# Kernel tuning notes

Hardware: AMD Instinct MI355X
Metric: run time of the kernel (lower is better)

Reference implementation:

```python
import jax, jax.numpy as jnp
import numpy as np

N = 50000      # nodes
E = 800000     # directed edges (avg degree 16)
D_IN = 128
D_HID = 128


def setup_inputs() -> dict:
    key = jax.random.key(0)
    k = jax.random.split(key, 6)
    x = jax.random.normal(k[0], (N, D_IN), dtype=jnp.float32)
    edge_index = jax.random.randint(k[1], (2, E), 0, N, dtype=jnp.int32)
    s = 1.0 / np.sqrt(D_IN)
    W1 = jax.random.normal(k[2], (D_IN, D_HID), dtype=jnp.float32) * s
    b1 = jnp.zeros((D_HID,), dtype=jnp.float32)
    W2 = jax.random.normal(k[3], (D_HID, D_HID), dtype=jnp.float32) * s
    b2 = jnp.zeros((D_HID,), dtype=jnp.float32)
    return {"x": x, "edge_index": edge_index, "W1": W1, "b1": b1, "W2": W2, "b2": b2}


def reference(x, edge_index, W1, b1, W2, b2):
    # PyG GCNConv default: add self-loops, symmetric normalization.
    src, dst = edge_index[0], edge_index[1]
    loop = jnp.arange(N, dtype=edge_index.dtype)
    s = jnp.concatenate([src, loop])   # [E+N] message sources
    d = jnp.concatenate([dst, loop])   # [E+N] message targets
    # degree on target nodes (incl. self-loops), edge weights = 1
    deg = jax.ops.segment_sum(jnp.ones_like(s, dtype=x.dtype), d, num_segments=N)
    dis = jnp.where(deg > 0, jax.lax.rsqrt(deg), 0.0)
    norm = dis[s] * dis[d]             # [E+N]

    def gcn_conv(h, W, b):
        h = h @ W                                           # [N, D]
        msg = h[s] * norm[:, None]                          # gather + per-edge scale
        return jax.ops.segment_sum(msg, d, num_segments=N) + b  # scatter-add + bias

    h = jax.nn.relu(gcn_conv(x, W1, b1))
    return gcn_conv(h, W2, b2)
```

## Files before the change

kernel.cpp:

```cpp
#include <hip/hip_runtime.h>

#define D 128
#define GBM 64
#define GBK 32


__global__ void k_count(const int* __restrict__ dst, int* __restrict__ cnt, int e) {
    int i = blockIdx.x * blockDim.x + threadIdx.x;
    if (i < e) atomicAdd(&cnt[dst[i]], 1);
}

__global__ __launch_bounds__(256) void k_scan1(const int* __restrict__ cnt,
                                               int* __restrict__ row_ptr,
                                               int* __restrict__ bsum,
                                               float* __restrict__ dis, int n) {
    __shared__ int s[256];
    int i = blockIdx.x * 256 + threadIdx.x;
    int v = (i < n) ? cnt[i] : 0;
    if (i < n) dis[i] = rsqrtf(1.0f + (float)v);
    s[threadIdx.x] = v;
    __syncthreads();
    for (int o = 1; o < 256; o <<= 1) {
        int t = (threadIdx.x >= o) ? s[threadIdx.x - o] : 0;
        __syncthreads();
        s[threadIdx.x] += t;
        __syncthreads();
    }
    if (i < n) row_ptr[i] = s[threadIdx.x] - v;
    if (threadIdx.x == 255) bsum[blockIdx.x] = s[255];
}

__global__ __launch_bounds__(256) void k_scan2(int* __restrict__ bsum, int nb) {
    __shared__ int s[256];
    int v = (threadIdx.x < nb) ? bsum[threadIdx.x] : 0;
    s[threadIdx.x] = v;
    __syncthreads();
    for (int o = 1; o < 256; o <<= 1) {
        int t = (threadIdx.x >= o) ? s[threadIdx.x - o] : 0;
        __syncthreads();
        s[threadIdx.x] += t;
        __syncthreads();
    }
    if (threadIdx.x < nb) bsum[threadIdx.x] = s[threadIdx.x] - v;
}

__global__ void k_scan3(int* __restrict__ row_ptr, const int* __restrict__ bsum, int n) {
    int i = blockIdx.x * 256 + threadIdx.x;
    if (i < n) row_ptr[i] += bsum[blockIdx.x];
}

__global__ void k_place(const int* __restrict__ ei, const int* __restrict__ row_ptr,
                        int* __restrict__ fill, int* __restrict__ srcs, int e) {
    int i = blockIdx.x * blockDim.x + threadIdx.x;
    if (i < e) {
        int s_ = ei[i];
        int d_ = ei[e + i];
        int pos = row_ptr[d_] + atomicAdd(&fill[d_], 1);
        srcs[pos] = s_;
    }
}


__global__ __launch_bounds__(256) void k_gemm_scale(
    const float* __restrict__ X, const float* __restrict__ W,
    const float* __restrict__ dis, float* __restrict__ Y, int nrows) {
    __shared__ float sA[GBK][GBM + 4];
    __shared__ float sB[GBK][D];
    int tid = threadIdx.x;
    int tx = tid & 15;
    int ty = tid >> 4;
    int row0 = blockIdx.x * GBM;

    float acc[4][8] = {};

    for (int kc = 0; kc < D; kc += GBK) {
        __syncthreads();
        #pragma unroll
        for (int jj = 0; jj < 2; ++jj) {
            int i = tid + jj * 256;
            int r = i >> 3;
            int kq = i & 7;
            int gr = row0 + r;
            float4 v = make_float4(0.f, 0.f, 0.f, 0.f);
            if (gr < nrows) v = *(const float4*)(X + (size_t)gr * D + kc + kq * 4);
            sA[kq * 4 + 0][r] = v.x;
            sA[kq * 4 + 1][r] = v.y;
            sA[kq * 4 + 2][r] = v.z;
            sA[kq * 4 + 3][r] = v.w;
        }
        #pragma unroll
        for (int jj = 0; jj < 4; ++jj) {
            int i = tid + jj * 256;
            int k = i >> 5;
            int nq = i & 31;
            *(float4*)(&sB[k][nq * 4]) = *(const float4*)(W + (size_t)(kc + k) * D + nq * 4);
        }
        __syncthreads();
        #pragma unroll
        for (int k = 0; k < GBK; ++k) {
            float a[4], b[8];
            *(float4*)&a[0] = *(float4*)&sA[k][ty * 4];
            *(float4*)&b[0] = *(float4*)&sB[k][tx * 4];
            *(float4*)&b[4] = *(float4*)&sB[k][tx * 4 + 64];
            #pragma unroll
            for (int i = 0; i < 4; ++i)
                #pragma unroll
                for (int j2 = 0; j2 < 8; ++j2)
                    acc[i][j2] += a[i] * b[j2];
        }
    }
    #pragma unroll
    for (int i = 0; i < 4; ++i) {
        int gr = row0 + ty * 4 + i;
        if (gr < nrows) {
            float dv = dis[gr];
            float4 o0, o1;
            o0.x = acc[i][0] * dv; o0.y = acc[i][1] * dv;
            o0.z = acc[i][2] * dv; o0.w = acc[i][3] * dv;
            o1.x = acc[i][4] * dv; o1.y = acc[i][5] * dv;
            o1.z = acc[i][6] * dv; o1.w = acc[i][7] * dv;
            *(float4*)(Y + (size_t)gr * D + tx * 4) = o0;
            *(float4*)(Y + (size_t)gr * D + tx * 4 + 64) = o1;
        }
    }
}


template <bool RELU>
__global__ __launch_bounds__(256) void k_aggregate(
    const float* __restrict__ g, const int* __restrict__ row_ptr,
    const int* __restrict__ cnt, const int* __restrict__ srcs,
    const float* __restrict__ dis, const float* __restrict__ b,
    float* __restrict__ out, int n) {
    long tid = (long)blockIdx.x * blockDim.x + threadIdx.x;
    int lane = (int)(tid & 31);
    int v = (int)(tid >> 5);
    if (v >= n) return;
    int beg = row_ptr[v];
    int c = cnt[v];
    const float4* g4 = (const float4*)g;
    float4 s0 = g4[(size_t)v * 32 + lane];
    float4 a0 = make_float4(0.f, 0.f, 0.f, 0.f);
    float4 a1 = a0, a2 = a0, a3 = a0;
    int j = 0;
    for (; j + 4 <= c; j += 4) {
        int u0 = srcs[beg + j + 0];
        int u1 = srcs[beg + j + 1];
        int u2 = srcs[beg + j + 2];
        int u3 = srcs[beg + j + 3];
        float4 t0 = g4[(size_t)u0 * 32 + lane];
        float4 t1 = g4[(size_t)u1 * 32 + lane];
        float4 t2 = g4[(size_t)u2 * 32 + lane];
        float4 t3 = g4[(size_t)u3 * 32 + lane];
        a0.x += t0.x; a0.y += t0.y; a0.z += t0.z; a0.w += t0.w;
        a1.x += t1.x; a1.y += t1.y; a1.z += t1.z; a1.w += t1.w;
        a2.x += t2.x; a2.y += t2.y; a2.z += t2.z; a2.w += t2.w;
        a3.x += t3.x; a3.y += t3.y; a3.z += t3.z; a3.w += t3.w;
    }
    for (; j < c; ++j) {
        int u = srcs[beg + j];
        float4 t = g4[(size_t)u * 32 + lane];
        a0.x += t.x; a0.y += t.y; a0.z += t.z; a0.w += t.w;
    }
    float4 acc;
    acc.x = s0.x + (a0.x + a1.x) + (a2.x + a3.x);
    acc.y = s0.y + (a0.y + a1.y) + (a2.y + a3.y);
    acc.z = s0.z + (a0.z + a1.z) + (a2.z + a3.z);
    acc.w = s0.w + (a0.w + a1.w) + (a2.w + a3.w);
    float dv = dis[v];
    float4 bb = ((const float4*)b)[lane];
    acc.x = acc.x * dv + bb.x;
    acc.y = acc.y * dv + bb.y;
    acc.z = acc.z * dv + bb.z;
    acc.w = acc.w * dv + bb.w;
    if (RELU) {
        acc.x = fmaxf(acc.x, 0.f);
        acc.y = fmaxf(acc.y, 0.f);
        acc.z = fmaxf(acc.z, 0.f);
        acc.w = fmaxf(acc.w, 0.f);
    }
    ((float4*)out)[(size_t)v * 32 + lane] = acc;
}


extern "C" void kernel_launch(void* const* d_in, const int* in_sizes, int n_in,
                              void* d_out, int out_size, void* d_ws, size_t ws_size,
                              hipStream_t stream) {
    const float* x  = (const float*)d_in[0];
    const int*   ei = (const int*)d_in[1];
    const float* W1 = (const float*)d_in[2];
    const float* b1 = (const float*)d_in[3];
    const float* W2 = (const float*)d_in[4];
    const float* b2 = (const float*)d_in[5];
    float* out = (float*)d_out;
    int n = in_sizes[0] / D;
    int e = in_sizes[1] / 2;

    char* p = (char*)d_ws;
    auto alloc = [&](size_t bytes) -> char* {
        char* r = p;
        p += (bytes + 255) & ~(size_t)255;
        return r;
    };
    int* cnt     = (int*)alloc((size_t)n * 4);
    int* fill    = (int*)alloc((size_t)n * 4);
    int* row_ptr = (int*)alloc((size_t)n * 4);
    int* bsum    = (int*)alloc(1024);
    float* dis   = (float*)alloc((size_t)n * 4);
    int* srcs    = (int*)alloc((size_t)e * 4);
    float* bufA  = (float*)alloc((size_t)n * D * 4);
    float* bufB  = (float*)alloc((size_t)n * D * 4);

    hipMemsetAsync(cnt, 0, (size_t)n * 4, stream);
    hipMemsetAsync(fill, 0, (size_t)n * 4, stream);

    int nb = (n + 255) / 256;
    k_count<<<(e + 255) / 256, 256, 0, stream>>>(ei + e, cnt, e);
    k_scan1<<<nb, 256, 0, stream>>>(cnt, row_ptr, bsum, dis, n);
    k_scan2<<<1, 256, 0, stream>>>(bsum, nb);
    k_scan3<<<nb, 256, 0, stream>>>(row_ptr, bsum, n);
    k_place<<<(e + 255) / 256, 256, 0, stream>>>(ei, row_ptr, fill, srcs, e);

    int gemm_blocks = (n + GBM - 1) / GBM;
    int agg_blocks = (int)(((long)n * 32 + 255) / 256);

    k_gemm_scale<<<gemm_blocks, 256, 0, stream>>>(x, W1, dis, bufA, n);
    k_aggregate<true><<<agg_blocks, 256, 0, stream>>>(bufA, row_ptr, cnt, srcs, dis, b1, bufB, n);
    k_gemm_scale<<<gemm_blocks, 256, 0, stream>>>(bufB, W2, dis, bufA, n);
    k_aggregate<false><<<agg_blocks, 256, 0, stream>>>(bufA, row_ptr, cnt, srcs, dis, b2, out, n);
}
```

Baseline: 343.2 us.

## Prefetch GEMM tiles in registers, fold scan fixup, widen aggregate unroll

Several unrelated changes at once. The GEMM now prefetches the next K-chunk of X and W into registers while the current chunk is computed, and gets a launch-bounds occupancy hint. The third scan kernel is dropped, so block offsets are added on the fly in placement and aggregation. The two memsets are merged into one, and the aggregate kernel unrolls by 8 with two accumulators and writes its output with nontemporal stores. Together these aim to hide GEMM load latency, remove two launches, and put more gathers in flight, at the cost of higher register pressure and an extra bsum read per node.

```diff
diff --git a/kernel.cpp b/kernel.cpp
--- a/kernel.cpp
+++ b/kernel.cpp
@@ -3,6 +3,8 @@
 #define D 128
 #define GBM 64
 #define GBK 32
+
+typedef float f32x4 __attribute__((ext_vector_type(4)));
 
 
 __global__ void k_count(const int* __restrict__ dst, int* __restrict__ cnt, int e) {
@@ -44,24 +46,20 @@
     if (threadIdx.x < nb) bsum[threadIdx.x] = s[threadIdx.x] - v;
 }
 
-__global__ void k_scan3(int* __restrict__ row_ptr, const int* __restrict__ bsum, int n) {
-    int i = blockIdx.x * 256 + threadIdx.x;
-    if (i < n) row_ptr[i] += bsum[blockIdx.x];
-}
-
 __global__ void k_place(const int* __restrict__ ei, const int* __restrict__ row_ptr,
+                        const int* __restrict__ bsum,
                         int* __restrict__ fill, int* __restrict__ srcs, int e) {
     int i = blockIdx.x * blockDim.x + threadIdx.x;
     if (i < e) {
         int s_ = ei[i];
         int d_ = ei[e + i];
-        int pos = row_ptr[d_] + atomicAdd(&fill[d_], 1);
+        int pos = row_ptr[d_] + bsum[d_ >> 8] + atomicAdd(&fill[d_], 1);
         srcs[pos] = s_;
     }
 }
 
 
-__global__ __launch_bounds__(256) void k_gemm_scale(
+__global__ __launch_bounds__(256, 4) void k_gemm_scale(
     const float* __restrict__ X, const float* __restrict__ W,
     const float* __restrict__ dis, float* __restrict__ Y, int nrows) {
     __shared__ float sA[GBK][GBM + 4];
@@ -71,31 +69,49 @@
     int ty = tid >> 4;
     int row0 = blockIdx.x * GBM;
 
+    int ar  = tid >> 3;
+    int akq = tid & 7;
+    int bk  = tid >> 5;
+    int bnq = tid & 31;
+
+    float4 ra0, ra1, rb0, rb1, rb2, rb3;
+    int gr0 = row0 + ar, gr1 = row0 + ar + 32;
+
+    ra0 = make_float4(0.f, 0.f, 0.f, 0.f); ra1 = ra0;
+    if (gr0 < nrows) ra0 = *(const float4*)(X + (size_t)gr0 * D + akq * 4);
+    if (gr1 < nrows) ra1 = *(const float4*)(X + (size_t)gr1 * D + akq * 4);
+    rb0 = *(const float4*)(W + (size_t)(bk     ) * D + bnq * 4);
+    rb1 = *(const float4*)(W + (size_t)(bk +  8) * D + bnq * 4);
+    rb2 = *(const float4*)(W + (size_t)(bk + 16) * D + bnq * 4);
+    rb3 = *(const float4*)(W + (size_t)(bk + 24) * D + bnq * 4);
+
     float acc[4][8] = {};
 
     for (int kc = 0; kc < D; kc += GBK) {
-        __syncthreads();
-        #pragma unroll
-        for (int jj = 0; jj < 2; ++jj) {
-            int i = tid + jj * 256;
-            int r = i >> 3;
-            int kq = i & 7;
-            int gr = row0 + r;
-            float4 v = make_float4(0.f, 0.f, 0.f, 0.f);
-            if (gr < nrows) v = *(const float4*)(X + (size_t)gr * D + kc + kq * 4);
-            sA[kq * 4 + 0][r] = v.x;
-            sA[kq * 4 + 1][r] = v.y;
-            sA[kq * 4 + 2][r] = v.z;
-            sA[kq * 4 + 3][r] = v.w;
+        if (kc) __syncthreads();
+        sA[akq * 4 + 0][ar]      = ra0.x;
+        sA[akq * 4 + 1][ar]      = ra0.y;
+        sA[akq * 4 + 2][ar]      = ra0.z;
+        sA[akq * 4 + 3][ar]      = ra0.w;
+        sA[akq * 4 + 0][ar + 32] = ra1.x;
+        sA[akq * 4 + 1][ar + 32] = ra1.y;
+        sA[akq * 4 + 2][ar + 32] = ra1.z;
+        sA[akq * 4 + 3][ar + 32] = ra1.w;
+        *(float4*)&sB[bk     ][bnq * 4] = rb0;
+        *(float4*)&sB[bk +  8][bnq * 4] = rb1;
+        *(float4*)&sB[bk + 16][bnq * 4] = rb2;
+        *(float4*)&sB[bk + 24][bnq * 4] = rb3;
+        __syncthreads();
+        int kn = kc + GBK;
+        if (kn < D) {
+            ra0 = make_float4(0.f, 0.f, 0.f, 0.f); ra1 = ra0;
+            if (gr0 < nrows) ra0 = *(const float4*)(X + (size_t)gr0 * D + kn + akq * 4);
+            if (gr1 < nrows) ra1 = *(const float4*)(X + (size_t)gr1 * D + kn + akq * 4);
+            rb0 = *(const float4*)(W + (size_t)(kn + bk     ) * D + bnq * 4);
+            rb1 = *(const float4*)(W + (size_t)(kn + bk +  8) * D + bnq * 4);
+            rb2 = *(const float4*)(W + (size_t)(kn + bk + 16) * D + bnq * 4);
+            rb3 = *(const float4*)(W + (size_t)(kn + bk + 24) * D + bnq * 4);
         }
-        #pragma unroll
-        for (int jj = 0; jj < 4; ++jj) {
-            int i = tid + jj * 256;
-            int k = i >> 5;
-            int nq = i & 31;
-            *(float4*)(&sB[k][nq * 4]) = *(const float4*)(W + (size_t)(kc + k) * D + nq * 4);
-        }
-        __syncthreads();
         #pragma unroll
         for (int k = 0; k < GBK; ++k) {
             float a[4], b[8];
@@ -129,44 +145,64 @@
 template <bool RELU>
 __global__ __launch_bounds__(256) void k_aggregate(
     const float* __restrict__ g, const int* __restrict__ row_ptr,
-    const int* __restrict__ cnt, const int* __restrict__ srcs,
-    const float* __restrict__ dis, const float* __restrict__ b,
-    float* __restrict__ out, int n) {
+    const int* __restrict__ bsum, const int* __restrict__ cnt,
+    const int* __restrict__ srcs, const float* __restrict__ dis,
+    const float* __restrict__ b, float* __restrict__ out, int n) {
     long tid = (long)blockIdx.x * blockDim.x + threadIdx.x;
     int lane = (int)(tid & 31);
     int v = (int)(tid >> 5);
     if (v >= n) return;
-    int beg = row_ptr[v];
+    int beg = row_ptr[v] + bsum[v >> 8];
     int c = cnt[v];
     const float4* g4 = (const float4*)g;
     float4 s0 = g4[(size_t)v * 32 + lane];
     float4 a0 = make_float4(0.f, 0.f, 0.f, 0.f);
-    float4 a1 = a0, a2 = a0, a3 = a0;
+    float4 a1 = a0;
     int j = 0;
-    for (; j + 4 <= c; j += 4) {
+    for (; j + 8 <= c; j += 8) {
         int u0 = srcs[beg + j + 0];
         int u1 = srcs[beg + j + 1];
         int u2 = srcs[beg + j + 2];
         int u3 = srcs[beg + j + 3];
+        int u4 = srcs[beg + j + 4];
+        int u5 = srcs[beg + j + 5];
+        int u6 = srcs[beg + j + 6];
+        int u7 = srcs[beg + j + 7];
         float4 t0 = g4[(size_t)u0 * 32 + lane];
         float4 t1 = g4[(size_t)u1 * 32 + lane];
         float4 t2 = g4[(size_t)u2 * 32 + lane];
         float4 t3 = g4[(size_t)u3 * 32 + lane];
+        float4 t4 = g4[(size_t)u4 * 32 + lane];
+        float4 t5 = g4[(size_t)u5 * 32 + lane];
+        float4 t6 = g4[(size_t)u6 * 32 + lane];
+        float4 t7 = g4[(size_t)u7 * 32 + lane];
         a0.x += t0.x; a0.y += t0.y; a0.z += t0.z; a0.w += t0.w;
         a1.x += t1.x; a1.y += t1.y; a1.z += t1.z; a1.w += t1.w;
-        a2.x += t2.x; a2.y += t2.y; a2.z += t2.z; a2.w += t2.w;
-        a3.x += t3.x; a3.y += t3.y; a3.z += t3.z; a3.w += t3.w;
-    }
-    for (; j < c; ++j) {
-        int u = srcs[beg + j];
-        float4 t = g4[(size_t)u * 32 + lane];
-        a0.x += t.x; a0.y += t.y; a0.z += t.z; a0.w += t.w;
+        a0.x += t2.x; a0.y += t2.y; a0.z += t2.z; a0.w += t2.w;
+        a1.x += t3.x; a1.y += t3.y; a1.z += t3.z; a1.w += t3.w;
+        a0.x += t4.x; a0.y += t4.y; a0.z += t4.z; a0.w += t4.w;
+        a1.x += t5.x; a1.y += t5.y; a1.z += t5.z; a1.w += t5.w;
+        a0.x += t6.x; a0.y += t6.y; a0.z += t6.z; a0.w += t6.w;
+        a1.x += t7.x; a1.y += t7.y; a1.z += t7.z; a1.w += t7.w;
+    }
+    for (; j + 2 <= c; j += 2) {
+        int u0 = srcs[beg + j + 0];
+        int u1 = srcs[beg + j + 1];
+        float4 t0 = g4[(size_t)u0 * 32 + lane];
+        float4 t1 = g4[(size_t)u1 * 32 + lane];
+        a0.x += t0.x; a0.y += t0.y; a0.z += t0.z; a0.w += t0.w;
+        a1.x += t1.x; a1.y += t1.y; a1.z += t1.z; a1.w += t1.w;
+    }
+    if (j < c) {
+        int u0 = srcs[beg + j];
+        float4 t0 = g4[(size_t)u0 * 32 + lane];
+        a0.x += t0.x; a0.y += t0.y; a0.z += t0.z; a0.w += t0.w;
     }
     float4 acc;
-    acc.x = s0.x + (a0.x + a1.x) + (a2.x + a3.x);
-    acc.y = s0.y + (a0.y + a1.y) + (a2.y + a3.y);
-    acc.z = s0.z + (a0.z + a1.z) + (a2.z + a3.z);
-    acc.w = s0.w + (a0.w + a1.w) + (a2.w + a3.w);
+    acc.x = s0.x + a0.x + a1.x;
+    acc.y = s0.y + a0.y + a1.y;
+    acc.z = s0.z + a0.z + a1.z;
+    acc.w = s0.w + a0.w + a1.w;
     float dv = dis[v];
     float4 bb = ((const float4*)b)[lane];
     acc.x = acc.x * dv + bb.x;
@@ -179,7 +215,8 @@
         acc.z = fmaxf(acc.z, 0.f);
         acc.w = fmaxf(acc.w, 0.f);
     }
-    ((float4*)out)[(size_t)v * 32 + lane] = acc;
+    f32x4 nv = {acc.x, acc.y, acc.z, acc.w};
+    __builtin_nontemporal_store(nv, (f32x4*)(out + (size_t)v * D + lane * 4));
 }
 
 
@@ -202,6 +239,7 @@
         p += (bytes + 255) & ~(size_t)255;
         return r;
     };
+    size_t na = (((size_t)n * 4) + 255) & ~(size_t)255;
     int* cnt     = (int*)alloc((size_t)n * 4);
     int* fill    = (int*)alloc((size_t)n * 4);
     int* row_ptr = (int*)alloc((size_t)n * 4);
@@ -211,21 +249,19 @@
     float* bufA  = (float*)alloc((size_t)n * D * 4);
     float* bufB  = (float*)alloc((size_t)n * D * 4);
 
-    hipMemsetAsync(cnt, 0, (size_t)n * 4, stream);
-    hipMemsetAsync(fill, 0, (size_t)n * 4, stream);
+    (void)hipMemsetAsync(cnt, 0, na * 2, stream);
 
     int nb = (n + 255) / 256;
     k_count<<<(e + 255) / 256, 256, 0, stream>>>(ei + e, cnt, e);
     k_scan1<<<nb, 256, 0, stream>>>(cnt, row_ptr, bsum, dis, n);
     k_scan2<<<1, 256, 0, stream>>>(bsum, nb);
-    k_scan3<<<nb, 256, 0, stream>>>(row_ptr, bsum, n);
-    k_place<<<(e + 255) / 256, 256, 0, stream>>>(ei, row_ptr, fill, srcs, e);
+    k_place<<<(e + 255) / 256, 256, 0, stream>>>(ei, row_ptr, bsum, fill, srcs, e);
 
     int gemm_blocks = (n + GBM - 1) / GBM;
     int agg_blocks = (int)(((long)n * 32 + 255) / 256);
 
     k_gemm_scale<<<gemm_blocks, 256, 0, stream>>>(x, W1, dis, bufA, n);
-    k_aggregate<true><<<agg_blocks, 256, 0, stream>>>(bufA, row_ptr, cnt, srcs, dis, b1, bufB, n);
+    k_aggregate<true><<<agg_blocks, 256, 0, stream>>>(bufA, row_ptr, bsum, cnt, srcs, dis, b1, bufB, n);
     k_gemm_scale<<<gemm_blocks, 256, 0, stream>>>(bufB, W2, dis, bufA, n);
-    k_aggregate<false><<<agg_blocks, 256, 0, stream>>>(bufA, row_ptr, cnt, srcs, dis, b2, out, n);
-}
+    k_aggregate<false><<<agg_blocks, 256, 0, stream>>>(bufA, row_ptr, bsum, cnt, srcs, dis, b2, out, n);
+}
```

New measurement: 339.6 us. No clear change (-1.1%).
